# Kernel optimization log

Hardware: AMD Instinct MI355X
Metric: run time of the kernel (lower is better)

## Reference

```python
import jax, jax.numpy as jnp
import numpy as np

N_TOKEN = 8192
N_EMBED = 512
N_SAMPLE = 10
TAU = 1.0
RHO = 1.0


def setup_inputs() -> dict:
    key = jax.random.key(0)
    k1, k2 = jax.random.split(key)
    inputs = jax.random.normal(k1, (4, 2048, N_EMBED), dtype=jnp.float32)
    embeds = jax.random.normal(k2, (N_TOKEN, N_EMBED), dtype=jnp.float32)
    return {"inputs": inputs, "embeds": embeds}


def reference(inputs, embeds):
    size = inputs.shape
    x = inputs.reshape(-1, N_EMBED)  # (N, D)
    n = x.shape[0]
    # squared distances, scaled by n_token (as in get_distances)
    dists = (jnp.sum(x * x, axis=-1, keepdims=True)
             + jnp.sum(embeds * embeds, axis=-1)[None, :]
             - 2.0 * jnp.matmul(x, embeds.T)) / N_TOKEN  # (N, K)
    logits = -dists / TAU  # categorical(softmax(logits)) == categorical(logits)
    skey = jax.random.fold_in(jax.random.key(0), 1)
    # multinomial with replacement: n_sample i.i.d. categorical draws per row
    samples = jax.random.categorical(skey, logits[:, None, :], axis=-1,
                                     shape=(n, N_SAMPLE))  # (N, n_sample) int
    quantized_embs = embeds[samples].mean(axis=1)  # (N, D) gather + mean
    quantized = x + jax.lax.stop_gradient(quantized_embs - x)  # straight-through
    gkey = jax.random.fold_in(jax.random.key(0), 2)
    gates = jax.random.bernoulli(gkey, RHO, (n,)).astype(x.dtype)[:, None]
    quantized = quantized * gates + (1.0 - gates) * x
    quantized = quantized.reshape(size)
    samples = samples.reshape(size[:-1] + (N_SAMPLE,))
    return quantized, samples
```

## Files before the change

kernel.cpp:

```cpp
#include <hip/hip_runtime.h>
#include <stdint.h>
#include <math.h>

#define N_ROWS 8192
#define N_TOK  8192
#define N_DIM  512
#define N_SAMP 10
#define GK     1536

typedef __attribute__((ext_vector_type(8))) short bf16x8_t;
typedef __attribute__((ext_vector_type(4))) float f32x4_t;

__host__ __device__ __forceinline__ void tf2x32(uint32_t ks0, uint32_t ks1,
                                                uint32_t& x0, uint32_t& x1) {
  uint32_t ks2 = ks0 ^ ks1 ^ 0x1BD11BDAu;
  x0 += ks0; x1 += ks1;
#define TF_ROUND(r) { x0 += x1; x1 = (x1 << (r)) | (x1 >> (32 - (r))); x1 ^= x0; }
  TF_ROUND(13) TF_ROUND(15) TF_ROUND(26) TF_ROUND(6)
  x0 += ks1; x1 += ks2 + 1u;
  TF_ROUND(17) TF_ROUND(29) TF_ROUND(16) TF_ROUND(24)
  x0 += ks2; x1 += ks0 + 2u;
  TF_ROUND(13) TF_ROUND(15) TF_ROUND(26) TF_ROUND(6)
  x0 += ks0; x1 += ks1 + 3u;
  TF_ROUND(17) TF_ROUND(29) TF_ROUND(16) TF_ROUND(24)
  x0 += ks1; x1 += ks2 + 4u;
  TF_ROUND(13) TF_ROUND(15) TF_ROUND(26) TF_ROUND(6)
  x0 += ks2; x1 += ks0 + 5u;
#undef TF_ROUND
}

__device__ __forceinline__ unsigned short f2bf_rne(float f) {
  uint32_t u = __float_as_uint(f);
  uint32_t r = (u + 0x7fffu + ((u >> 16) & 1u)) >> 16;
  return (unsigned short)r;
}
__device__ __forceinline__ float bf2f(unsigned short h) {
  return __uint_as_float((uint32_t)h << 16);
}

__global__ __launch_bounds__(256) void rownorm_kernel(const float* __restrict__ M,
                                                      float* __restrict__ out) {
  int lane = threadIdx.x & 63;
  int row = (int)((blockIdx.x * blockDim.x + threadIdx.x) >> 6);
  const float* p = M + (size_t)row * N_DIM;
  float acc = 0.f;
#pragma unroll
  for (int d = 0; d < N_DIM; d += 64) {
    float v = p[d + lane];
    acc = fmaf(v, v, acc);
  }
#pragma unroll
  for (int off = 32; off; off >>= 1) acc += __shfl_xor(acc, off, 64);
  if (lane == 0) out[row] = acc;
}

__global__ __launch_bounds__(256) void init_state_kernel(float* __restrict__ rmax,
                                                         int* __restrict__ ridx) {
  int i = blockIdx.x * 256 + threadIdx.x;
  if (i < N_ROWS * N_SAMP) { rmax[i] = -INFINITY; ridx[i] = 0; }
}

__global__ __launch_bounds__(256) void split_kernel(const float* __restrict__ src,
                                                    unsigned short* __restrict__ dst,
                                                    int mode) {
  int t = blockIdx.x * 256 + threadIdx.x;
  int row = t >> 7;
  int c = (t & 127) << 2;
  float4 v = *(const float4*)(src + (size_t)row * N_DIM + c);
  ushort4 hi, lo;
  hi.x = f2bf_rne(v.x); lo.x = f2bf_rne(v.x - bf2f(hi.x));
  hi.y = f2bf_rne(v.y); lo.y = f2bf_rne(v.y - bf2f(hi.y));
  hi.z = f2bf_rne(v.z); lo.z = f2bf_rne(v.z - bf2f(hi.z));
  hi.w = f2bf_rne(v.w); lo.w = f2bf_rne(v.w - bf2f(hi.w));
  unsigned short* base = dst + (size_t)row * GK;
  *(ushort4*)(base + c) = hi;
  if (mode == 0) {
    *(ushort4*)(base + 512 + c) = lo;
    *(ushort4*)(base + 1024 + c) = hi;
  } else {
    *(ushort4*)(base + 512 + c) = hi;
    *(ushort4*)(base + 1024 + c) = lo;
  }
}

__global__ __launch_bounds__(256) void gemm_bf16_kernel(const unsigned short* __restrict__ A2,
                                                        const unsigned short* __restrict__ B2,
                                                        float* __restrict__ C,
                                                        int ks, int KC) {
  __shared__ __align__(16) unsigned short As[128 * 32];
  __shared__ __align__(16) unsigned short Bs[128 * 32];
  int tid = threadIdx.x;
  int w = tid >> 6, l = tid & 63;
  int row0 = blockIdx.y * 128;
  int col0 = blockIdx.x * 128;
  int bcol0 = ks + col0;
  int wm = (w & 1) * 64, wn = (w >> 1) * 64;
  int quad = l >> 4, r15 = l & 15;

  f32x4_t acc[4][4];
#pragma unroll
  for (int i = 0; i < 4; ++i)
#pragma unroll
    for (int j = 0; j < 4; ++j) acc[i][j] = (f32x4_t){0.f, 0.f, 0.f, 0.f};

  int c0 = w * 64 + l;
  int c1 = c0 + 256;
  const size_t ga0 = (size_t)(row0 + (c0 >> 2)) * GK + (c0 & 3) * 8;
  const size_t ga1 = (size_t)(row0 + (c1 >> 2)) * GK + (c1 & 3) * 8;
  const size_t gb0 = (size_t)(bcol0 + (c0 >> 2)) * GK + (c0 & 3) * 8;
  const size_t gb1 = (size_t)(bcol0 + (c1 >> 2)) * GK + (c1 & 3) * 8;

  for (int k0 = 0; k0 < GK; k0 += 32) {
    uint4 ra0 = *(const uint4*)(A2 + ga0 + k0);
    uint4 ra1 = *(const uint4*)(A2 + ga1 + k0);
    uint4 rb0 = *(const uint4*)(B2 + gb0 + k0);
    uint4 rb1 = *(const uint4*)(B2 + gb1 + k0);
    __syncthreads();
    *(uint4*)(As + c0 * 8) = ra0;
    *(uint4*)(As + c1 * 8) = ra1;
    *(uint4*)(Bs + c0 * 8) = rb0;
    *(uint4*)(Bs + c1 * 8) = rb1;
    __syncthreads();

    bf16x8_t af[4], bf[4];
#pragma unroll
    for (int i = 0; i < 4; ++i)
      af[i] = *(const bf16x8_t*)&As[(wm + i * 16 + r15) * 32 + quad * 8];
#pragma unroll
    for (int j = 0; j < 4; ++j)
      bf[j] = *(const bf16x8_t*)&Bs[(wn + j * 16 + r15) * 32 + quad * 8];
#pragma unroll
    for (int i = 0; i < 4; ++i)
#pragma unroll
      for (int j = 0; j < 4; ++j)
        acc[i][j] = __builtin_amdgcn_mfma_f32_16x16x32_bf16(af[i], bf[j], acc[i][j], 0, 0, 0);
  }

#pragma unroll
  for (int i = 0; i < 4; ++i)
#pragma unroll
    for (int j = 0; j < 4; ++j) {
#pragma unroll
      for (int r = 0; r < 4; ++r) {
        int grow = row0 + wm + i * 16 + quad * 4 + r;
        int gcol = col0 + wn + j * 16 + r15;
        C[(size_t)grow * KC + gcol] = acc[i][j][r];
      }
    }
}

__global__ __launch_bounds__(256) void gemm_nt_kernel(const float* __restrict__ A,
                                                      const float* __restrict__ B,
                                                      float* __restrict__ C,
                                                      int ks, int KC) {
  __shared__ __align__(16) float Asf[32][68];
  __shared__ __align__(16) float Bsf[32][68];
  int tid = threadIdx.x;
  int row0 = blockIdx.y * 64;
  int colB0 = blockIdx.x * 64 + ks;
  int tx = tid & 15, ty = tid >> 4;
  float acc[4][4] = {};
  for (int d0 = 0; d0 < N_DIM; d0 += 32) {
#pragma unroll
    for (int r = 0; r < 2; ++r) {
      int c = tid + 256 * r;
      int m = c >> 3;
      int dv = (c & 7) << 2;
      const float4 va = *(const float4*)(A + (size_t)(row0 + m) * N_DIM + d0 + dv);
      Asf[dv + 0][m] = va.x; Asf[dv + 1][m] = va.y;
      Asf[dv + 2][m] = va.z; Asf[dv + 3][m] = va.w;
      const float4 vb = *(const float4*)(B + (size_t)(colB0 + m) * N_DIM + d0 + dv);
      Bsf[dv + 0][m] = vb.x; Bsf[dv + 1][m] = vb.y;
      Bsf[dv + 2][m] = vb.z; Bsf[dv + 3][m] = vb.w;
    }
    __syncthreads();
#pragma unroll
    for (int dd = 0; dd < 32; ++dd) {
      float4 a4 = *(const float4*)&Asf[dd][ty << 2];
      float4 b4 = *(const float4*)&Bsf[dd][tx << 2];
      float av[4] = {a4.x, a4.y, a4.z, a4.w};
      float bv[4] = {b4.x, b4.y, b4.z, b4.w};
#pragma unroll
      for (int i = 0; i < 4; ++i)
#pragma unroll
        for (int j = 0; j < 4; ++j)
          acc[i][j] = fmaf(av[i], bv[j], acc[i][j]);
    }
    __syncthreads();
  }
  int colC0 = blockIdx.x * 64;
#pragma unroll
  for (int i = 0; i < 4; ++i) {
    float4 v = make_float4(acc[i][0], acc[i][1], acc[i][2], acc[i][3]);
    *(float4*)(C + (size_t)(row0 + (ty << 2) + i) * KC + colC0 + (tx << 2)) = v;
  }
}

__global__ __launch_bounds__(256) void sample_kernel(const float* __restrict__ dots,
                                                     const float* __restrict__ xx,
                                                     const float* __restrict__ ee,
                                                     float* __restrict__ rmax,
                                                     int* __restrict__ ridx,
                                                     int ks, int KC,
                                                     uint32_t k0, uint32_t k1) {
  int lane = threadIdx.x & 63;
  int row = (int)((blockIdx.x * blockDim.x + threadIdx.x) >> 6);
  float xxi = xx[row];
  float bmax[N_SAMP];
  int bidx[N_SAMP];
#pragma unroll
  for (int s = 0; s < N_SAMP; ++s) { bmax[s] = -INFINITY; bidx[s] = 0; }
  const float inv_nt = 1.f / 8192.f;
  const float tiny = 1.1754943508222875e-38f;
  uint32_t rowbase = (uint32_t)row * (uint32_t)N_SAMP;

  for (int kk = lane; kk < KC; kk += 64) {
    int k = ks + kk;
    float dot = dots[(size_t)row * KC + kk];
    float t = xxi + ee[k];
    float L = (2.f * dot - t) * inv_nt;
#pragma unroll
    for (int s = 0; s < N_SAMP; ++s) {
      uint32_t c = (rowbase + (uint32_t)s) * 8192u + (uint32_t)k;
      uint32_t x0 = 0u, x1 = c;
      tf2x32(k0, k1, x0, x1);
      uint32_t bits = x0 ^ x1;
      float u = __uint_as_float(0x3f800000u | (bits >> 9)) - 1.0f;
      u = u + tiny;
      u = fmaxf(tiny, u);
      float g = -logf(-logf(u));
      float v = g + L;
      if (v > bmax[s]) { bmax[s] = v; bidx[s] = k; }
    }
  }
#pragma unroll
  for (int s = 0; s < N_SAMP; ++s) {
    float v = bmax[s];
    int id = bidx[s];
#pragma unroll
    for (int off = 32; off; off >>= 1) {
      float ov = __shfl_xor(v, off, 64);
      int oi = __shfl_xor(id, off, 64);
      if (ov > v || (ov == v && oi < id)) { v = ov; id = oi; }
    }
    if (lane == 0) {
      size_t p = (size_t)row * N_SAMP + s;
      if (v > rmax[p]) { rmax[p] = v; ridx[p] = id; }
    }
  }
}

__global__ __launch_bounds__(256) void gather_kernel(const float* __restrict__ emb,
                                                     const int* __restrict__ ridx,
                                                     const float* __restrict__ x,
                                                     float* __restrict__ outq,
                                                     float* __restrict__ outs) {
  int lane = threadIdx.x & 63;
  int row = (int)((blockIdx.x * blockDim.x + threadIdx.x) >> 6);
  int idx[N_SAMP];
#pragma unroll
  for (int s = 0; s < N_SAMP; ++s) idx[s] = ridx[row * N_SAMP + s];
  if (lane < N_SAMP) outs[row * N_SAMP + lane] = (float)idx[lane];
#pragma unroll
  for (int c = lane; c < N_DIM; c += 64) {
    float sum = 0.f;
#pragma unroll
    for (int s = 0; s < N_SAMP; ++s) sum += emb[(size_t)idx[s] * N_DIM + c];
    float qe = sum / 10.0f;
    float xv = x[(size_t)row * N_DIM + c];
    outq[(size_t)row * N_DIM + c] = xv + (qe - xv);
  }
}

extern "C" void kernel_launch(void* const* d_in, const int* in_sizes, int n_in,
                              void* d_out, int out_size, void* d_ws, size_t ws_size,
                              hipStream_t stream) {
  const float* x = (const float*)d_in[0];
  const float* emb = (const float*)d_in[1];
  float* out_q = (float*)d_out;
  float* out_s = out_q + (size_t)N_ROWS * N_DIM;

  const size_t fixed_f = (size_t)N_ROWS + N_TOK + 2 * (size_t)N_ROWS * N_SAMP;
  const size_t out_f = (size_t)N_ROWS * N_DIM + (size_t)N_ROWS * N_SAMP;
  const size_t split_u = (size_t)N_ROWS * GK;

  uint32_t s0 = 0u, s1 = 1u;
  tf2x32(0u, 0u, s0, s1);

  int KC = 0;
  for (int c = 8192; c >= 128; c >>= 1) {
    size_t need = fixed_f * 4 + 2 * split_u * 2 + (size_t)N_ROWS * c * 4;
    if (need <= ws_size) { KC = c; break; }
  }

  if (KC) {
    float* xx = (float*)d_ws;
    float* ee = xx + N_ROWS;
    float* rmax = ee + N_TOK;
    int* ridx = (int*)(rmax + (size_t)N_ROWS * N_SAMP);
    unsigned short* A2 = (unsigned short*)(ridx + (size_t)N_ROWS * N_SAMP);
    unsigned short* B2 = A2 + split_u;
    float* dots = (float*)(B2 + split_u);

    rownorm_kernel<<<2048, 256, 0, stream>>>(x, xx);
    rownorm_kernel<<<2048, 256, 0, stream>>>(emb, ee);
    init_state_kernel<<<(N_ROWS * N_SAMP + 255) / 256, 256, 0, stream>>>(rmax, ridx);
    split_kernel<<<N_ROWS * 128 / 256, 256, 0, stream>>>(x, A2, 0);
    split_kernel<<<N_ROWS * 128 / 256, 256, 0, stream>>>(emb, B2, 1);

    for (int ks = 0; ks < N_TOK; ks += KC) {
      gemm_bf16_kernel<<<dim3(KC / 128, N_ROWS / 128), 256, 0, stream>>>(A2, B2, dots, ks, KC);
      sample_kernel<<<2048, 256, 0, stream>>>(dots, xx, ee, rmax, ridx, ks, KC, s0, s1);
    }
    gather_kernel<<<2048, 256, 0, stream>>>(emb, ridx, x, out_q, out_s);
    return;
  }

  float *xx, *ee, *rmax, *dots;
  int* ridx;
  KC = 0;
  for (int c = 8192; c >= 64; c >>= 1) {
    if ((fixed_f + (size_t)N_ROWS * c) * 4 <= ws_size) { KC = c; break; }
  }
  if (KC) {
    xx = (float*)d_ws;
    ee = xx + N_ROWS;
    rmax = ee + N_TOK;
    ridx = (int*)(rmax + (size_t)N_ROWS * N_SAMP);
    dots = (float*)(ridx + (size_t)N_ROWS * N_SAMP);
  } else if (fixed_f * 4 <= ws_size) {
    KC = 512;
    xx = (float*)d_ws;
    ee = xx + N_ROWS;
    rmax = ee + N_TOK;
    ridx = (int*)(rmax + (size_t)N_ROWS * N_SAMP);
    dots = out_q;
  } else {
    KC = 256;
    dots = out_q;
    float* tail = out_q + (out_f - fixed_f);
    xx = tail;
    ee = xx + N_ROWS;
    rmax = ee + N_TOK;
    ridx = (int*)(rmax + (size_t)N_ROWS * N_SAMP);
  }

  rownorm_kernel<<<2048, 256, 0, stream>>>(x, xx);
  rownorm_kernel<<<2048, 256, 0, stream>>>(emb, ee);
  init_state_kernel<<<(N_ROWS * N_SAMP + 255) / 256, 256, 0, stream>>>(rmax, ridx);
  for (int ks = 0; ks < N_TOK; ks += KC) {
    gemm_nt_kernel<<<dim3(KC / 64, N_ROWS / 64), 256, 0, stream>>>(x, emb, dots, ks, KC);
    sample_kernel<<<2048, 256, 0, stream>>>(dots, xx, ee, rmax, ridx, ks, KC, s0, s1);
  }
  gather_kernel<<<2048, 256, 0, stream>>>(emb, ridx, x, out_q, out_s);
}
```

Before: 1.876 ms.

## Replace Gumbel-max with exponential-race sampling, fuse distance epilogue into GEMM

The sampler switches from Gumbel-max (two logs per draw) to an equivalent exponential race: the GEMM epilogue writes exp(dist) per entry, and the sampler minimises -log(u)*E, so each of the ten draws needs one log instead of two. The distance computation (norms, scale) moves into the GEMM epilogue, and the bf16 GEMM loads tiles with global_load_lds direct-to-LDS copies. The risks are that exp of the distance may overflow or lose precision in ways that change which indices win, and that the tiny-value handling of u differs from before, so sample indices may diverge from the reference.

```diff
diff --git a/kernel.cpp b/kernel.cpp
--- a/kernel.cpp
+++ b/kernel.cpp
@@ -54,10 +54,10 @@
   if (lane == 0) out[row] = acc;
 }
 
-__global__ __launch_bounds__(256) void init_state_kernel(float* __restrict__ rmax,
+__global__ __launch_bounds__(256) void init_state_kernel(float* __restrict__ rmin,
                                                          int* __restrict__ ridx) {
   int i = blockIdx.x * 256 + threadIdx.x;
-  if (i < N_ROWS * N_SAMP) { rmax[i] = -INFINITY; ridx[i] = 0; }
+  if (i < N_ROWS * N_SAMP) { rmin[i] = INFINITY; ridx[i] = 0; }
 }
 
 __global__ __launch_bounds__(256) void split_kernel(const float* __restrict__ src,
@@ -83,9 +83,16 @@
   }
 }
 
+__device__ __forceinline__ void async_cp16(const void* g, void* l) {
+  __builtin_amdgcn_global_load_lds((const __attribute__((address_space(1))) void*)g,
+                                   (__attribute__((address_space(3))) void*)l, 16, 0, 0);
+}
+
 __global__ __launch_bounds__(256) void gemm_bf16_kernel(const unsigned short* __restrict__ A2,
                                                         const unsigned short* __restrict__ B2,
-                                                        float* __restrict__ C,
+                                                        const float* __restrict__ xx,
+                                                        const float* __restrict__ ee,
+                                                        float* __restrict__ E,
                                                         int ks, int KC) {
   __shared__ __align__(16) unsigned short As[128 * 32];
   __shared__ __align__(16) unsigned short Bs[128 * 32];
@@ -111,15 +118,10 @@
   const size_t gb1 = (size_t)(bcol0 + (c1 >> 2)) * GK + (c1 & 3) * 8;
 
   for (int k0 = 0; k0 < GK; k0 += 32) {
-    uint4 ra0 = *(const uint4*)(A2 + ga0 + k0);
-    uint4 ra1 = *(const uint4*)(A2 + ga1 + k0);
-    uint4 rb0 = *(const uint4*)(B2 + gb0 + k0);
-    uint4 rb1 = *(const uint4*)(B2 + gb1 + k0);
-    __syncthreads();
-    *(uint4*)(As + c0 * 8) = ra0;
-    *(uint4*)(As + c1 * 8) = ra1;
-    *(uint4*)(Bs + c0 * 8) = rb0;
-    *(uint4*)(Bs + c1 * 8) = rb1;
+    async_cp16(A2 + ga0 + k0, As + c0 * 8);
+    async_cp16(A2 + ga1 + k0, As + c1 * 8);
+    async_cp16(B2 + gb0 + k0, Bs + c0 * 8);
+    async_cp16(B2 + gb1 + k0, Bs + c1 * 8);
     __syncthreads();
 
     bf16x8_t af[4], bf[4];
@@ -134,24 +136,34 @@
 #pragma unroll
       for (int j = 0; j < 4; ++j)
         acc[i][j] = __builtin_amdgcn_mfma_f32_16x16x32_bf16(af[i], bf[j], acc[i][j], 0, 0, 0);
-  }
-
-#pragma unroll
-  for (int i = 0; i < 4; ++i)
-#pragma unroll
-    for (int j = 0; j < 4; ++j) {
-#pragma unroll
-      for (int r = 0; r < 4; ++r) {
-        int grow = row0 + wm + i * 16 + quad * 4 + r;
+    __syncthreads();
+  }
+
+  const float inv_nt = 1.f / 8192.f;
+  float eev[4];
+#pragma unroll
+  for (int j = 0; j < 4; ++j) eev[j] = ee[ks + col0 + wn + j * 16 + r15];
+#pragma unroll
+  for (int i = 0; i < 4; ++i) {
+#pragma unroll
+    for (int r = 0; r < 4; ++r) {
+      int grow = row0 + wm + i * 16 + quad * 4 + r;
+      float xxv = xx[grow];
+#pragma unroll
+      for (int j = 0; j < 4; ++j) {
         int gcol = col0 + wn + j * 16 + r15;
-        C[(size_t)grow * KC + gcol] = acc[i][j][r];
+        float dist = (xxv + eev[j] - 2.0f * acc[i][j][r]) * inv_nt;
+        E[(size_t)grow * KC + gcol] = expf(dist);
       }
     }
+  }
 }
 
 __global__ __launch_bounds__(256) void gemm_nt_kernel(const float* __restrict__ A,
                                                       const float* __restrict__ B,
-                                                      float* __restrict__ C,
+                                                      const float* __restrict__ xx,
+                                                      const float* __restrict__ ee,
+                                                      float* __restrict__ E,
                                                       int ks, int KC) {
   __shared__ __align__(16) float Asf[32][68];
   __shared__ __align__(16) float Bsf[32][68];
@@ -188,64 +200,66 @@
     }
     __syncthreads();
   }
+  const float inv_nt = 1.f / 8192.f;
   int colC0 = blockIdx.x * 64;
+  float eev[4];
+#pragma unroll
+  for (int j = 0; j < 4; ++j) eev[j] = ee[ks + colC0 + (tx << 2) + j];
 #pragma unroll
   for (int i = 0; i < 4; ++i) {
-    float4 v = make_float4(acc[i][0], acc[i][1], acc[i][2], acc[i][3]);
-    *(float4*)(C + (size_t)(row0 + (ty << 2) + i) * KC + colC0 + (tx << 2)) = v;
-  }
-}
-
-__global__ __launch_bounds__(256) void sample_kernel(const float* __restrict__ dots,
-                                                     const float* __restrict__ xx,
-                                                     const float* __restrict__ ee,
-                                                     float* __restrict__ rmax,
+    int grow = row0 + (ty << 2) + i;
+    float xxv = xx[grow];
+    float4 v;
+    v.x = expf((xxv + eev[0] - 2.0f * acc[i][0]) * inv_nt);
+    v.y = expf((xxv + eev[1] - 2.0f * acc[i][1]) * inv_nt);
+    v.z = expf((xxv + eev[2] - 2.0f * acc[i][2]) * inv_nt);
+    v.w = expf((xxv + eev[3] - 2.0f * acc[i][3]) * inv_nt);
+    *(float4*)(E + (size_t)grow * KC + colC0 + (tx << 2)) = v;
+  }
+}
+
+__global__ __launch_bounds__(256) void sample_kernel(const float* __restrict__ E,
+                                                     float* __restrict__ rmin,
                                                      int* __restrict__ ridx,
                                                      int ks, int KC,
                                                      uint32_t k0, uint32_t k1) {
   int lane = threadIdx.x & 63;
   int row = (int)((blockIdx.x * blockDim.x + threadIdx.x) >> 6);
-  float xxi = xx[row];
-  float bmax[N_SAMP];
+  float bmin[N_SAMP];
   int bidx[N_SAMP];
 #pragma unroll
-  for (int s = 0; s < N_SAMP; ++s) { bmax[s] = -INFINITY; bidx[s] = 0; }
-  const float inv_nt = 1.f / 8192.f;
+  for (int s = 0; s < N_SAMP; ++s) { bmin[s] = INFINITY; bidx[s] = 0; }
   const float tiny = 1.1754943508222875e-38f;
-  uint32_t rowbase = (uint32_t)row * (uint32_t)N_SAMP;
+  uint32_t row_c = (uint32_t)row * (uint32_t)N_SAMP * 8192u;
 
   for (int kk = lane; kk < KC; kk += 64) {
     int k = ks + kk;
-    float dot = dots[(size_t)row * KC + kk];
-    float t = xxi + ee[k];
-    float L = (2.f * dot - t) * inv_nt;
+    float Ek = E[(size_t)row * KC + kk];
+    uint32_t base_c = row_c + (uint32_t)k;
 #pragma unroll
     for (int s = 0; s < N_SAMP; ++s) {
-      uint32_t c = (rowbase + (uint32_t)s) * 8192u + (uint32_t)k;
-      uint32_t x0 = 0u, x1 = c;
+      uint32_t x0 = 0u, x1 = base_c + (uint32_t)s * 8192u;
       tf2x32(k0, k1, x0, x1);
       uint32_t bits = x0 ^ x1;
       float u = __uint_as_float(0x3f800000u | (bits >> 9)) - 1.0f;
-      u = u + tiny;
-      u = fmaxf(tiny, u);
-      float g = -logf(-logf(u));
-      float v = g + L;
-      if (v > bmax[s]) { bmax[s] = v; bidx[s] = k; }
+      u = fmaxf(u, tiny);
+      float wv = -logf(u) * Ek;
+      if (wv < bmin[s]) { bmin[s] = wv; bidx[s] = k; }
     }
   }
 #pragma unroll
   for (int s = 0; s < N_SAMP; ++s) {
-    float v = bmax[s];
+    float v = bmin[s];
     int id = bidx[s];
 #pragma unroll
     for (int off = 32; off; off >>= 1) {
       float ov = __shfl_xor(v, off, 64);
       int oi = __shfl_xor(id, off, 64);
-      if (ov > v || (ov == v && oi < id)) { v = ov; id = oi; }
+      if (ov < v || (ov == v && oi < id)) { v = ov; id = oi; }
     }
     if (lane == 0) {
       size_t p = (size_t)row * N_SAMP + s;
-      if (v > rmax[p]) { rmax[p] = v; ridx[p] = id; }
+      if (v < rmin[p]) { rmin[p] = v; ridx[p] = id; }
     }
   }
 }
@@ -296,27 +310,27 @@
   if (KC) {
     float* xx = (float*)d_ws;
     float* ee = xx + N_ROWS;
-    float* rmax = ee + N_TOK;
-    int* ridx = (int*)(rmax + (size_t)N_ROWS * N_SAMP);
+    float* rmin = ee + N_TOK;
+    int* ridx = (int*)(rmin + (size_t)N_ROWS * N_SAMP);
     unsigned short* A2 = (unsigned short*)(ridx + (size_t)N_ROWS * N_SAMP);
     unsigned short* B2 = A2 + split_u;
-    float* dots = (float*)(B2 + split_u);
+    float* E = (float*)(B2 + split_u);
 
     rownorm_kernel<<<2048, 256, 0, stream>>>(x, xx);
     rownorm_kernel<<<2048, 256, 0, stream>>>(emb, ee);
-    init_state_kernel<<<(N_ROWS * N_SAMP + 255) / 256, 256, 0, stream>>>(rmax, ridx);
+    init_state_kernel<<<(N_ROWS * N_SAMP + 255) / 256, 256, 0, stream>>>(rmin, ridx);
     split_kernel<<<N_ROWS * 128 / 256, 256, 0, stream>>>(x, A2, 0);
     split_kernel<<<N_ROWS * 128 / 256, 256, 0, stream>>>(emb, B2, 1);
 
     for (int ks = 0; ks < N_TOK; ks += KC) {
-      gemm_bf16_kernel<<<dim3(KC / 128, N_ROWS / 128), 256, 0, stream>>>(A2, B2, dots, ks, KC);
-      sample_kernel<<<2048, 256, 0, stream>>>(dots, xx, ee, rmax, ridx, ks, KC, s0, s1);
+      gemm_bf16_kernel<<<dim3(KC / 128, N_ROWS / 128), 256, 0, stream>>>(A2, B2, xx, ee, E, ks, KC);
+      sample_kernel<<<2048, 256, 0, stream>>>(E, rmin, ridx, ks, KC, s0, s1);
     }
     gather_kernel<<<2048, 256, 0, stream>>>(emb, ridx, x, out_q, out_s);
     return;
   }
 
-  float *xx, *ee, *rmax, *dots;
+  float *xx, *ee, *rmin, *E;
   int* ridx;
   KC = 0;
   for (int c = 8192; c >= 64; c >>= 1) {
@@ -325,32 +339,32 @@
   if (KC) {
     xx = (float*)d_ws;
     ee = xx + N_ROWS;
-    rmax = ee + N_TOK;
-    ridx = (int*)(rmax + (size_t)N_ROWS * N_SAMP);
-    dots = (float*)(ridx + (size_t)N_ROWS * N_SAMP);
+    rmin = ee + N_TOK;
+    ridx = (int*)(rmin + (size_t)N_ROWS * N_SAMP);
+    E = (float*)(ridx + (size_t)N_ROWS * N_SAMP);
   } else if (fixed_f * 4 <= ws_size) {
     KC = 512;
     xx = (float*)d_ws;
     ee = xx + N_ROWS;
-    rmax = ee + N_TOK;
-    ridx = (int*)(rmax + (size_t)N_ROWS * N_SAMP);
-    dots = out_q;
+    rmin = ee + N_TOK;
+    ridx = (int*)(rmin + (size_t)N_ROWS * N_SAMP);
+    E = out_q;
   } else {
     KC = 256;
-    dots = out_q;
+    E = out_q;
     float* tail = out_q + (out_f - fixed_f);
     xx = tail;
     ee = xx + N_ROWS;
-    rmax = ee + N_TOK;
-    ridx = (int*)(rmax + (size_t)N_ROWS * N_SAMP);
+    rmin = ee + N_TOK;
+    ridx = (int*)(rmin + (size_t)N_ROWS * N_SAMP);
   }
 
   rownorm_kernel<<<2048, 256, 0, stream>>>(x, xx);
   rownorm_kernel<<<2048, 256, 0, stream>>>(emb, ee);
-  init_state_kernel<<<(N_ROWS * N_SAMP + 255) / 256, 256, 0, stream>>>(rmax, ridx);
+  init_state_kernel<<<(N_ROWS * N_SAMP + 255) / 256, 256, 0, stream>>>(rmin, ridx);
   for (int ks = 0; ks < N_TOK; ks += KC) {
-    gemm_nt_kernel<<<dim3(KC / 64, N_ROWS / 64), 256, 0, stream>>>(x, emb, dots, ks, KC);
-    sample_kernel<<<2048, 256, 0, stream>>>(dots, xx, ee, rmax, ridx, ks, KC, s0, s1);
+    gemm_nt_kernel<<<dim3(KC / 64, N_ROWS / 64), 256, 0, stream>>>(x, emb, xx, ee, E, ks, KC);
+    sample_kernel<<<2048, 256, 0, stream>>>(E, rmin, ridx, ks, KC, s0, s1);
   }
   gather_kernel<<<2048, 256, 0, stream>>>(emb, ridx, x, out_q, out_s);
 }
```

Result: faster. 1.724 ms (-8.1%).
